# Kernel tuning notes

Measured on AMD Instinct MI355X. Metric: run time of the kernel, lower is better.

The kernel has to match this reference:

```python
import jax, jax.numpy as jnp
import numpy as np
from jax import lax

B, CIN, COUT, H, W = 4, 256, 256, 64, 64
KH = KW = 3
STRIDE = PAD = DIL = 1
GROUPS = 1
K = KH * KW
HO = (H + 2 * PAD - DIL * (KH - 1) - 1) // STRIDE + 1
WO = (W + 2 * PAD - DIL * (KW - 1) - 1) // STRIDE + 1
DN = ('NCHW', 'OIHW', 'NCHW')


def _sep_conv(x, dw, pw):
    # Separable2d: depthwise kxk conv (stride/pad/dilation) then pointwise 1x1.
    y = lax.conv_general_dilated(x, dw, (STRIDE, STRIDE), [(PAD, PAD), (PAD, PAD)],
                                 rhs_dilation=(DIL, DIL), feature_group_count=x.shape[1],
                                 dimension_numbers=DN)
    return lax.conv_general_dilated(y, pw, (1, 1), 'VALID', dimension_numbers=DN)


def _deform_conv2d(x, offset, mask, weight, bias):
    Bb, Cin, Hh, Ww = x.shape
    O = weight.shape[0]
    G = offset.shape[1] // (2 * K)  # offset groups
    offs = offset.reshape(Bb, G, K, 2, HO, WO)
    dy, dx = offs[:, :, :, 0], offs[:, :, :, 1]  # [B,G,K,Ho,Wo]
    ki, kj = jnp.meshgrid(jnp.arange(KH), jnp.arange(KW), indexing='ij')
    base_y = (-PAD + ki.reshape(K, 1) * DIL + jnp.arange(HO)[None, :] * STRIDE).astype(x.dtype)  # [K,Ho]
    base_x = (-PAD + kj.reshape(K, 1) * DIL + jnp.arange(WO)[None, :] * STRIDE).astype(x.dtype)  # [K,Wo]
    py = base_y[None, None, :, :, None] + dy  # [B,G,K,Ho,Wo]
    px = base_x[None, None, :, None, :] + dx

    xg = x.reshape(Bb, G, Cin // G, Hh, Ww)

    def bilinear(img, py, px):
        # img [C,H,W], py/px [K,Ho,Wo]; zero-padding outside bounds.
        y0 = jnp.floor(py)
        x0 = jnp.floor(px)
        out = jnp.zeros((img.shape[0],) + py.shape, img.dtype)
        for a, (iy, wy) in enumerate((((y0), (y0 + 1 - py)), ((y0 + 1), (py - y0)))):
            for b, (ix, wx) in enumerate((((x0), (x0 + 1 - px)), ((x0 + 1), (px - x0)))):
                valid = (iy >= 0) & (iy < Hh) & (ix >= 0) & (ix < Ww)
                iyc = jnp.clip(iy, 0, Hh - 1).astype(jnp.int32)
                ixc = jnp.clip(ix, 0, Ww - 1).astype(jnp.int32)
                v = img[:, iyc, ixc]  # [C,K,Ho,Wo]
                out = out + v * (wy * wx * valid)[None]
        return out

    sampled = jax.vmap(jax.vmap(bilinear))(xg, py, px)  # [B,G,C/G,K,Ho,Wo]
    m = mask.reshape(Bb, G, K, HO, WO)
    sampled = sampled * m[:, :, None]

    cols = sampled.reshape(Bb, Cin, K, HO, WO).reshape(Bb, GROUPS, Cin // GROUPS, K, HO, WO)
    wr = weight.reshape(GROUPS, O // GROUPS, Cin // GROUPS, K)
    out = jnp.einsum('bgckhw,gock->bgohw', cols, wr).reshape(Bb, O, HO, WO)
    return out + bias[None, :, None, None]


def setup_inputs() -> dict:
    key = jax.random.key(0)
    ks = jax.random.split(key, 7)
    x = jax.random.normal(ks[0], (B, CIN, H, W), jnp.float32)
    weight = jax.random.normal(ks[1], (COUT, CIN // GROUPS, KH, KW), jnp.float32) / np.sqrt(CIN * K)
    bias = jax.random.normal(ks[2], (COUT,), jnp.float32) * 0.01
    off_dw = jax.random.normal(ks[3], (CIN, 1, KH, KW), jnp.float32) * 0.01
    off_pw = jax.random.normal(ks[4], (2 * K * GROUPS, CIN, 1, 1), jnp.float32) * 0.01
    mask_dw = jax.random.normal(ks[5], (CIN, 1, KH, KW), jnp.float32) * 0.01
    mask_pw = jax.random.normal(ks[6], (K * GROUPS, CIN, 1, 1), jnp.float32) * 0.01
    return dict(x=x, weight=weight, bias=bias, off_dw=off_dw, off_pw=off_pw,
                mask_dw=mask_dw, mask_pw=mask_pw)


def reference(x, weight, bias, off_dw, off_pw, mask_dw, mask_pw):
    offset = _sep_conv(x, off_dw, off_pw)                       # [B,2*K,Ho,Wo]
    mask = jax.nn.sigmoid(_sep_conv(x, mask_dw, mask_pw)) * 2.0  # MaskSigmoid(scale=2)
    return _deform_conv2d(x, offset, mask, weight, bias)
```

## Files before the change

### kernel.cpp

```cpp
#include <hip/hip_runtime.h>

#define CIN   256
#define COUT  256
#define HH    64
#define WW    64
#define KD    2304
#define NPIX  16384
#define SPLIT 16
#define CPS   (CIN / SPLIT)

typedef __attribute__((ext_vector_type(8))) short  short8v;
typedef __attribute__((ext_vector_type(4))) float  float4v;
typedef __attribute__((ext_vector_type(4))) unsigned short ushort4v;
typedef __attribute__((ext_vector_type(2))) unsigned int uint2v;
typedef unsigned int u32;
typedef unsigned short u16;

__device__ __forceinline__ u16 f2bf(float f) {
  union { float f; unsigned u; } v; v.f = f;
  unsigned r = v.u + 0x7FFFu + ((v.u >> 16) & 1u);
  return (u16)(r >> 16);
}
__device__ __forceinline__ float bf2f(u16 h) {
  union { unsigned u; float f; } v; v.u = ((unsigned)h) << 16;
  return v.f;
}

__device__ __forceinline__ void gload_lds16(const void* g, void* l) {
  __builtin_amdgcn_global_load_lds((const __attribute__((address_space(1))) u32*)g,
                                   (__attribute__((address_space(3))) u32*)l, 16, 0, 0);
}

__global__ __launch_bounds__(256) void offmask_part_kernel(
    const float* __restrict__ x,
    const float* __restrict__ off_dw, const float* __restrict__ off_pw,
    const float* __restrict__ mask_dw, const float* __restrict__ mask_pw,
    float* __restrict__ part)
{
  int m = blockIdx.x * 256 + threadIdx.x;
  int s = blockIdx.y;
  int b = m >> 12, pix = m & 4095;
  int ho = pix >> 6, wo = pix & 63;
  const float* xb = x + (size_t)b * CIN * 4096;

  float acc[27];
#pragma unroll
  for (int j = 0; j < 27; ++j) acc[j] = 0.f;

  int c0 = s * CPS;
  for (int ci = 0; ci < CPS; ++ci) {
    int c = c0 + ci;
    const float* xc = xb + (size_t)c * 4096;
    float d_off = 0.f, d_msk = 0.f;
#pragma unroll
    for (int t = 0; t < 9; ++t) {
      int gy = ho + t / 3 - 1, gx = wo + t % 3 - 1;
      bool ok = (gy >= 0) & (gy < HH) & (gx >= 0) & (gx < WW);
      float v = ok ? xc[gy * 64 + gx] : 0.f;
      d_off += v * off_dw[c * 9 + t];
      d_msk += v * mask_dw[c * 9 + t];
    }
#pragma unroll
    for (int j = 0; j < 18; ++j) acc[j] += d_off * off_pw[j * 256 + c];
#pragma unroll
    for (int j = 0; j < 9; ++j) acc[18 + j] += d_msk * mask_pw[j * 256 + c];
  }
  float* pp = part + ((size_t)s * NPIX + m) * 32;
#pragma unroll
  for (int j = 0; j < 27; ++j) pp[j] = acc[j];
}

__global__ __launch_bounds__(256) void offmask_reduce_kernel(
    const float* __restrict__ part, float* __restrict__ rec)
{
  int i = blockIdx.x * 256 + threadIdx.x;
  int m = i >> 5, j = i & 31;
  if (j >= 27) { rec[i] = 0.f; return; }
  float sum = 0.f;
#pragma unroll
  for (int s = 0; s < SPLIT; ++s) sum += part[((size_t)s * NPIX + m) * 32 + j];
  rec[i] = (j < 18) ? sum : 2.f / (1.f + __expf(-sum));
}

__global__ __launch_bounds__(256) void wconv_kernel(const float* __restrict__ w,
                                                    u16* __restrict__ wb)
{
  int i = blockIdx.x * 256 + threadIdx.x;
  int co = i / KD, rem = i - co * KD;
  int c = rem / 9, kk = rem - c * 9;
  wb[co * KD + kk * 256 + c] = f2bf(w[i]);
}

__global__ __launch_bounds__(256) void xpose_kernel(const float* __restrict__ x,
                                                    u16* __restrict__ xt)
{
  __shared__ float t[64][65];
  int ptile = blockIdx.x;
  int ctile = blockIdx.y;
  int b     = blockIdx.z;
  int tid = threadIdx.x;
  const float* xb = x + (size_t)b * CIN * 4096 + (size_t)ctile * 64 * 4096 + ptile * 64;
#pragma unroll
  for (int i = 0; i < 16; ++i) {
    int c = i * 4 + (tid >> 6), p = tid & 63;
    t[c][p] = xb[(size_t)c * 4096 + p];
  }
  __syncthreads();
  u16* xo = xt + ((size_t)b * 4096 + ptile * 64) * 256 + ctile * 64;
#pragma unroll
  for (int i = 0; i < 16; ++i) {
    int p = i * 4 + (tid >> 6), c = tid & 63;
    xo[(size_t)p * 256 + c] = f2bf(t[c][p]);
  }
}

__global__ __launch_bounds__(512) void gemm_fused_kernel(
    const u16* __restrict__ A,
    const u16* __restrict__ xt,
    const float* __restrict__ rec,
    const float* __restrict__ bias,
    float* __restrict__ out)
{
  __shared__ __align__(16) u16 lA[2][256 * 32];
  __shared__ __align__(16) u16 lB[2][64 * 32];
  const int tid = threadIdx.x;
  const int bid = blockIdx.x;
  const int m0  = bid * 64;
  const int b_img = bid >> 6;
  const int wave = tid >> 6, lane = tid & 63;
  const int wm = wave >> 1, wn = wave & 1;
  const int rl = lane & 15, kq = lane >> 4;
  const int sA = (kq ^ (rl & 3) ^ ((rl >> 2) & 3)) * 8;

  const int rA  = tid >> 2;
  const int koA = ((tid & 3) ^ (rA & 3) ^ ((rA >> 2) & 3)) * 8;
  const u16* aRow0 = A + (size_t)rA * KD + koA;
  const u16* aRow1 = A + (size_t)(rA + 128) * KD + koA;

  const int spx = tid >> 3;
  const int sc4 = (tid & 7) * 4;
  const int m_px = m0 + spx;
  const int ho = (m_px & 4095) >> 6, wo = m_px & 63;
  const float* rp = rec + (size_t)m_px * 32;
  const u16* xb = xt + (size_t)b_img * 4096 * 256;
  const int wAddr = spx * 32 +
                    ((((tid >> 1) & 3) ^ ((spx & 3) ^ ((spx >> 2) & 3))) * 8) +
                    (tid & 1) * 4;

  u32 cOff[4];
  float cW[4];

#define CALC_CORNERS(kk_) do {                                             \
    float dy = rp[(kk_) * 2], dx = rp[(kk_) * 2 + 1], msk = rp[18 + (kk_)];\
    float py  = (float)(ho - 1 + ((kk_) / 3)) + dy;                        \
    float pxf = (float)(wo - 1 + ((kk_) % 3)) + dx;                        \
    float fy = floorf(py), fx = floorf(pxf);                               \
    int y0 = (int)fy, x0 = (int)fx;                                        \
    float wy1 = py - fy, wy0 = 1.f - wy1;                                  \
    float wx1 = pxf - fx, wx0 = 1.f - wx1;                                 \
    _Pragma("unroll")                                                      \
    for (int cr = 0; cr < 4; ++cr) {                                       \
      int iy = y0 + (cr >> 1), ix = x0 + (cr & 1);                         \
      bool valid = (iy >= 0) & (iy < HH) & (ix >= 0) & (ix < WW);          \
      int iyc = min(max(iy, 0), HH - 1), ixc = min(max(ix, 0), WW - 1);    \
      cOff[cr] = (u32)(iyc * 64 + ixc) * 256;                              \
      float wy = (cr >> 1) ? wy1 : wy0;                                    \
      float wx = (cr & 1) ? wx1 : wx0;                                     \
      cW[cr] = valid ? (wy * wx * msk) : 0.f;                              \
    }                                                                      \
  } while (0)

#define STAGE_A(t, bufi) do {                                              \
    int k0_ = (t) * 32;                                                    \
    gload_lds16(aRow0 + k0_, lA[bufi] + tid * 8);                          \
    gload_lds16(aRow1 + k0_, lA[bufi] + (tid + 512) * 8);                  \
  } while (0)

  float4v acc[4][2];
#pragma unroll
  for (int m = 0; m < 4; ++m)
#pragma unroll
    for (int n = 0; n < 2; ++n) acc[m][n] = float4v{0.f, 0.f, 0.f, 0.f};

  {
    CALC_CORNERS(0);
    ushort4v v0 = *(const ushort4v*)(xb + cOff[0] + sc4);
    ushort4v v1 = *(const ushort4v*)(xb + cOff[1] + sc4);
    ushort4v v2 = *(const ushort4v*)(xb + cOff[2] + sc4);
    ushort4v v3 = *(const ushort4v*)(xb + cOff[3] + sc4);
    float a0 = cW[0]*bf2f(v0[0]) + cW[1]*bf2f(v1[0]) + cW[2]*bf2f(v2[0]) + cW[3]*bf2f(v3[0]);
    float a1 = cW[0]*bf2f(v0[1]) + cW[1]*bf2f(v1[1]) + cW[2]*bf2f(v2[1]) + cW[3]*bf2f(v3[1]);
    float a2 = cW[0]*bf2f(v0[2]) + cW[1]*bf2f(v1[2]) + cW[2]*bf2f(v2[2]) + cW[3]*bf2f(v3[2]);
    float a3 = cW[0]*bf2f(v0[3]) + cW[1]*bf2f(v1[3]) + cW[2]*bf2f(v2[3]) + cW[3]*bf2f(v3[3]);
    uint2v wv;
    wv[0] = (u32)f2bf(a0) | ((u32)f2bf(a1) << 16);
    wv[1] = (u32)f2bf(a2) | ((u32)f2bf(a3) << 16);
    *(uint2v*)&lB[0][wAddr] = wv;
    STAGE_A(0, 0);
  }
  __syncthreads();

#pragma unroll 2
  for (int ks = 0; ks < 72; ++ks) {
    const int cur = ks & 1;
    ushort4v v0, v1, v2, v3;
    const bool have = (ks < 71);
    if (have) {
      STAGE_A(ks + 1, cur ^ 1);
      int ksn = ks + 1;
      if ((ksn & 7) == 0) CALC_CORNERS(ksn >> 3);
      int c0n = (ksn & 7) * 32;
      v0 = *(const ushort4v*)(xb + cOff[0] + c0n + sc4);
      v1 = *(const ushort4v*)(xb + cOff[1] + c0n + sc4);
      v2 = *(const ushort4v*)(xb + cOff[2] + c0n + sc4);
      v3 = *(const ushort4v*)(xb + cOff[3] + c0n + sc4);
    }
    short8v af[4], bf[2];
#pragma unroll
    for (int m = 0; m < 4; ++m)
      af[m] = *(const short8v*)&lA[cur][(wm * 64 + m * 16 + rl) * 32 + sA];
#pragma unroll
    for (int n = 0; n < 2; ++n)
      bf[n] = *(const short8v*)&lB[cur][(wn * 32 + n * 16 + rl) * 32 + sA];
#pragma unroll
    for (int m = 0; m < 4; ++m)
#pragma unroll
      for (int n = 0; n < 2; ++n)
        acc[m][n] = __builtin_amdgcn_mfma_f32_16x16x32_bf16(af[m], bf[n], acc[m][n], 0, 0, 0);
    if (have) {
      float a0 = cW[0]*bf2f(v0[0]) + cW[1]*bf2f(v1[0]) + cW[2]*bf2f(v2[0]) + cW[3]*bf2f(v3[0]);
      float a1 = cW[0]*bf2f(v0[1]) + cW[1]*bf2f(v1[1]) + cW[2]*bf2f(v2[1]) + cW[3]*bf2f(v3[1]);
      float a2 = cW[0]*bf2f(v0[2]) + cW[1]*bf2f(v1[2]) + cW[2]*bf2f(v2[2]) + cW[3]*bf2f(v3[2]);
      float a3 = cW[0]*bf2f(v0[3]) + cW[1]*bf2f(v1[3]) + cW[2]*bf2f(v2[3]) + cW[3]*bf2f(v3[3]);
      uint2v wv;
      wv[0] = (u32)f2bf(a0) | ((u32)f2bf(a1) << 16);
      wv[1] = (u32)f2bf(a2) | ((u32)f2bf(a3) << 16);
      *(uint2v*)&lB[cur ^ 1][wAddr] = wv;
    }
    __syncthreads();
  }
#undef STAGE_A
#undef CALC_CORNERS

  const int p_base = (m0 & 4095) + wn * 32;
  float* ob = out + (size_t)b_img * COUT * 4096;
#pragma unroll
  for (int m = 0; m < 4; ++m) {
#pragma unroll
    for (int j = 0; j < 4; ++j) {
      int co = wm * 64 + m * 16 + kq * 4 + j;
      float bv = bias[co];
#pragma unroll
      for (int n = 0; n < 2; ++n) {
        int pp = p_base + n * 16 + rl;
        ob[(size_t)co * 4096 + pp] = acc[m][n][j] + bv;
      }
    }
  }
}

extern "C" void kernel_launch(void* const* d_in, const int* in_sizes, int n_in,
                              void* d_out, int out_size, void* d_ws, size_t ws_size,
                              hipStream_t stream) {
  const float* x       = (const float*)d_in[0];
  const float* weight  = (const float*)d_in[1];
  const float* bias    = (const float*)d_in[2];
  const float* off_dw  = (const float*)d_in[3];
  const float* off_pw  = (const float*)d_in[4];
  const float* mask_dw = (const float*)d_in[5];
  const float* mask_pw = (const float*)d_in[6];

  if (ws_size < 45219840ull) return;
  float* rec  = (float*)d_ws;
  u16*   wb   = (u16*)((char*)d_ws + 2097152);
  u16*   xt   = (u16*)((char*)d_ws + 3276800);
  float* part = (float*)((char*)d_ws + 11665408);
  float* out  = (float*)d_out;

  wconv_kernel<<<dim3(2304), dim3(256), 0, stream>>>(weight, wb);
  offmask_part_kernel<<<dim3(NPIX / 256, SPLIT), dim3(256), 0, stream>>>(
      x, off_dw, off_pw, mask_dw, mask_pw, part);
  offmask_reduce_kernel<<<dim3(NPIX * 32 / 256), dim3(256), 0, stream>>>(part, rec);
  xpose_kernel<<<dim3(64, 4, 4), dim3(256), 0, stream>>>(x, xt);
  gemm_fused_kernel<<<dim3(256), dim3(512), 0, stream>>>(wb, xt, rec, bias, out);
}
```

Before: 113.1 us.

## Split GEMM reduction over channel halves and add partial outputs

The fused deformable GEMM is split along the input-channel dimension into two halves, doubling the block count so each CU can hold more waves. The second half writes its partial sums to a workspace buffer (reusing the offset/mask partials area), and a new elementwise kernel adds it into the output. This trades extra global memory traffic and an additional launch for more parallelism and latency hiding in the gather-heavy GEMM.

```diff
diff --git a/kernel.cpp b/kernel.cpp
--- a/kernel.cpp
+++ b/kernel.cpp
@@ -119,14 +119,18 @@
     const u16* __restrict__ xt,
     const float* __restrict__ rec,
     const float* __restrict__ bias,
-    float* __restrict__ out)
+    float* __restrict__ out,
+    float* __restrict__ tmp)
 {
   __shared__ __align__(16) u16 lA[2][256 * 32];
   __shared__ __align__(16) u16 lB[2][64 * 32];
   const int tid = threadIdx.x;
   const int bid = blockIdx.x;
-  const int m0  = bid * 64;
-  const int b_img = bid >> 6;
+  const int h   = bid & 1;
+  const int ptile = bid >> 1;
+  const int m0  = ptile * 64;
+  const int b_img = ptile >> 6;
+  const int cbase = h * 128;
   const int wave = tid >> 6, lane = tid & 63;
   const int wm = wave >> 1, wn = wave & 1;
   const int rl = lane & 15, kq = lane >> 4;
@@ -149,6 +153,8 @@
 
   u32 cOff[4];
   float cW[4];
+
+#define KCOL(t_) (((t_) >> 2) * 256 + cbase + ((t_) & 3) * 32)
 
 #define CALC_CORNERS(kk_) do {                                             \
     float dy = rp[(kk_) * 2], dx = rp[(kk_) * 2 + 1], msk = rp[18 + (kk_)];\
@@ -171,7 +177,7 @@
   } while (0)
 
 #define STAGE_A(t, bufi) do {                                              \
-    int k0_ = (t) * 32;                                                    \
+    int k0_ = KCOL(t);                                                     \
     gload_lds16(aRow0 + k0_, lA[bufi] + tid * 8);                          \
     gload_lds16(aRow1 + k0_, lA[bufi] + (tid + 512) * 8);                  \
   } while (0)
@@ -184,10 +190,11 @@
 
   {
     CALC_CORNERS(0);
-    ushort4v v0 = *(const ushort4v*)(xb + cOff[0] + sc4);
-    ushort4v v1 = *(const ushort4v*)(xb + cOff[1] + sc4);
-    ushort4v v2 = *(const ushort4v*)(xb + cOff[2] + sc4);
-    ushort4v v3 = *(const ushort4v*)(xb + cOff[3] + sc4);
+    int c0n = cbase + sc4;
+    ushort4v v0 = *(const ushort4v*)(xb + cOff[0] + c0n);
+    ushort4v v1 = *(const ushort4v*)(xb + cOff[1] + c0n);
+    ushort4v v2 = *(const ushort4v*)(xb + cOff[2] + c0n);
+    ushort4v v3 = *(const ushort4v*)(xb + cOff[3] + c0n);
     float a0 = cW[0]*bf2f(v0[0]) + cW[1]*bf2f(v1[0]) + cW[2]*bf2f(v2[0]) + cW[3]*bf2f(v3[0]);
     float a1 = cW[0]*bf2f(v0[1]) + cW[1]*bf2f(v1[1]) + cW[2]*bf2f(v2[1]) + cW[3]*bf2f(v3[1]);
     float a2 = cW[0]*bf2f(v0[2]) + cW[1]*bf2f(v1[2]) + cW[2]*bf2f(v2[2]) + cW[3]*bf2f(v3[2]);
@@ -200,20 +207,20 @@
   }
   __syncthreads();
 
-#pragma unroll 2
-  for (int ks = 0; ks < 72; ++ks) {
+#pragma unroll 4
+  for (int ks = 0; ks < 36; ++ks) {
     const int cur = ks & 1;
     ushort4v v0, v1, v2, v3;
-    const bool have = (ks < 71);
+    const bool have = (ks < 35);
     if (have) {
       STAGE_A(ks + 1, cur ^ 1);
       int ksn = ks + 1;
-      if ((ksn & 7) == 0) CALC_CORNERS(ksn >> 3);
-      int c0n = (ksn & 7) * 32;
-      v0 = *(const ushort4v*)(xb + cOff[0] + c0n + sc4);
-      v1 = *(const ushort4v*)(xb + cOff[1] + c0n + sc4);
-      v2 = *(const ushort4v*)(xb + cOff[2] + c0n + sc4);
-      v3 = *(const ushort4v*)(xb + cOff[3] + c0n + sc4);
+      if ((ksn & 3) == 0) CALC_CORNERS(ksn >> 2);
+      int c0n = cbase + (ksn & 3) * 32 + sc4;
+      v0 = *(const ushort4v*)(xb + cOff[0] + c0n);
+      v1 = *(const ushort4v*)(xb + cOff[1] + c0n);
+      v2 = *(const ushort4v*)(xb + cOff[2] + c0n);
+      v3 = *(const ushort4v*)(xb + cOff[3] + c0n);
     }
     short8v af[4], bf[2];
 #pragma unroll
@@ -241,22 +248,33 @@
   }
 #undef STAGE_A
 #undef CALC_CORNERS
+#undef KCOL
 
   const int p_base = (m0 & 4095) + wn * 32;
-  float* ob = out + (size_t)b_img * COUT * 4096;
+  float* db = (h ? tmp : out) + (size_t)b_img * COUT * 4096;
 #pragma unroll
   for (int m = 0; m < 4; ++m) {
 #pragma unroll
     for (int j = 0; j < 4; ++j) {
       int co = wm * 64 + m * 16 + kq * 4 + j;
-      float bv = bias[co];
+      float bv = h ? 0.f : bias[co];
 #pragma unroll
       for (int n = 0; n < 2; ++n) {
         int pp = p_base + n * 16 + rl;
-        ob[(size_t)co * 4096 + pp] = acc[m][n][j] + bv;
+        db[(size_t)co * 4096 + pp] = acc[m][n][j] + bv;
       }
     }
   }
+}
+
+__global__ __launch_bounds__(256) void add_kernel(float* __restrict__ out,
+                                                  const float* __restrict__ tmp)
+{
+  int i = blockIdx.x * 256 + threadIdx.x;
+  float4v a = *(const float4v*)(out + (size_t)i * 4);
+  float4v b = *(const float4v*)(tmp + (size_t)i * 4);
+  a += b;
+  *(float4v*)(out + (size_t)i * 4) = a;
 }
 
 extern "C" void kernel_launch(void* const* d_in, const int* in_sizes, int n_in,
@@ -275,6 +293,7 @@
   u16*   wb   = (u16*)((char*)d_ws + 2097152);
   u16*   xt   = (u16*)((char*)d_ws + 3276800);
   float* part = (float*)((char*)d_ws + 11665408);
+  float* tmp  = part;
   float* out  = (float*)d_out;
 
   wconv_kernel<<<dim3(2304), dim3(256), 0, stream>>>(weight, wb);
@@ -282,5 +301,6 @@
       x, off_dw, off_pw, mask_dw, mask_pw, part);
   offmask_reduce_kernel<<<dim3(NPIX * 32 / 256), dim3(256), 0, stream>>>(part, rec);
   xpose_kernel<<<dim3(64, 4, 4), dim3(256), 0, stream>>>(x, xt);
-  gemm_fused_kernel<<<dim3(256), dim3(512), 0, stream>>>(wb, xt, rec, bias, out);
-}
+  gemm_fused_kernel<<<dim3(512), dim3(512), 0, stream>>>(wb, xt, rec, bias, out, tmp);
+  add_kernel<<<dim3((COUT * NPIX / 4) / 256), dim3(256), 0, stream>>>(out, tmp);
+}
```

After: 106.5 us. -5.8%, faster.
